# Performance work log

Measured on AMD Instinct MI355X. Metric: run time of the kernel, lower is better.

Reference implementation:

```python
import jax, jax.numpy as jnp
import numpy as np

NEG_BIG = -9.0e15  # matches torch's -9000000000000000.0 mask fill
ALPHA = 0.2        # leakyrelu negative slope


def setup_inputs() -> dict:
    key = jax.random.key(0)
    k1, k2, k3, k4, k5 = jax.random.split(key, 5)
    N, F_in, F_out = 4096, 512, 64
    stdv = 1.0 / np.sqrt(F_out)
    x = jax.random.normal(k1, (N, F_in), dtype=jnp.float32)
    adj = jax.random.randint(k2, (N, N), 0, 2, dtype=jnp.int32)
    W = jax.random.uniform(k3, (F_in, F_out), dtype=jnp.float32, minval=-stdv, maxval=stdv)
    a = jax.random.normal(k4, (2 * F_out, 1), dtype=jnp.float32) * 0.1
    bias = jax.random.uniform(k5, (F_out,), dtype=jnp.float32, minval=-stdv, maxval=stdv)
    return {"x": x, "adj": adj, "W": W, "a": a, "bias": bias}


def _gat_forward(x, adj, W, a, bias):
    N = x.shape[0]
    F_out = W.shape[1]
    h = x @ W  # (N, F)
    a1 = a[:F_out, 0]   # weights hitting the first concat half
    a2 = a[F_out:, 0]   # weights hitting the second concat half
    # First half: row k=i*N+j of the concat holds h_j  ->  e1[j] = h_j . a1
    e1 = h @ a1  # (N,)
    # Second half of this repo's concat is NOT h_i; exact index algebra:
    # second[k=i*N+j, r] = h[(r*N+i)//F, (((r*N+i)%F)*N + j) % F]
    # Since it depends on j only via j % F, build table T[i, t] (t = j % F).
    r = jnp.arange(F_out)[:, None]          # (F, 1)
    i = jnp.arange(N)[None, :]              # (1, N)
    m = r * N + i                           # (F, N)
    p = m // F_out                          # row index into h
    s0 = m % F_out
    t = jnp.arange(F_out)                   # (F,)
    col = (s0[..., None] * N + t) % F_out   # (F, N, F) column index into h
    vals = h[p[..., None], col]             # (F, N, F)
    T = jnp.einsum('r,rit->it', a2, vals)   # (N, F)
    j = jnp.arange(N)
    e2 = T[:, j % F_out]                    # (N, N) second-half contribution
    e = e1[None, :] + e2                    # (N, N) pre-activation scores
    e = jnp.where(e > 0, e, ALPHA * e)      # LeakyReLU(0.2)
    e = jnp.where(adj > 0, e, NEG_BIG)      # mask non-edges
    att = jax.nn.softmax(e, axis=1)         # row-wise softmax (dropout = eval identity)
    out = jax.nn.relu(att @ h) + bias       # relu BEFORE bias add, as in source
    return out


def reference(x, adj, W, a, bias):
    return _gat_forward(x, adj, W, a, bias)
```

## Files before the change

kernel.cpp:

```cpp
#include <hip/hip_runtime.h>
#include <math.h>

#define N_NODES 4096
#define F_IN    512
#define F_OUT   64
#define ALPHA   0.2f
#define NPART   8

typedef _Float16 half8 __attribute__((ext_vector_type(8)));
typedef _Float16 half4 __attribute__((ext_vector_type(4)));
typedef float    floatx4 __attribute__((ext_vector_type(4)));

union H8U4 { half8 h; uint32_t u[4]; };

__device__ __forceinline__ void async_copy16(void* lds, const void* g) {
    __builtin_amdgcn_global_load_lds(
        (const __attribute__((address_space(1))) unsigned int*)g,
        (__attribute__((address_space(3))) unsigned int*)lds, 16, 0, 0);
}

__global__ __launch_bounds__(256) void k_prep(const float* __restrict__ W,
                                              _Float16* __restrict__ WT) {
    int idx = blockIdx.x * 256 + threadIdx.x;
    int t = idx >> 9;
    int k = idx & 511;
    WT[idx] = (_Float16)W[k * F_OUT + t];
}

__global__ __launch_bounds__(512) void k_hW(const float* __restrict__ x,
                                            const _Float16* __restrict__ WT,
                                            const float* __restrict__ a,
                                            float* __restrict__ h,
                                            _Float16* __restrict__ hT,
                                            float* __restrict__ e1) {
    __shared__ float red[8][16][64];
    int tid  = threadIdx.x;
    int lane = tid & 63;
    int w    = tid >> 6;
    int i0   = blockIdx.x * 16;
    int n    = lane & 15;
    int quad = lane >> 4;

    floatx4 acc[4] = {{0,0,0,0},{0,0,0,0},{0,0,0,0},{0,0,0,0}};

    const float* xr = x + (size_t)(i0 + n) * F_IN + w * 64 + quad * 8;
    const _Float16* wb = WT + w * 64 + quad * 8;
#pragma unroll
    for (int kk = 0; kk < 64; kk += 32) {
        float4 x0 = *(const float4*)(xr + kk);
        float4 x1 = *(const float4*)(xr + kk + 4);
        half8 af = {(_Float16)x0.x, (_Float16)x0.y, (_Float16)x0.z, (_Float16)x0.w,
                    (_Float16)x1.x, (_Float16)x1.y, (_Float16)x1.z, (_Float16)x1.w};
#pragma unroll
        for (int g = 0; g < 4; ++g) {
            half8 bf = *(const half8*)(wb + (size_t)(g * 16 + n) * F_IN + kk);
            acc[g] = __builtin_amdgcn_mfma_f32_16x16x32_f16(af, bf, acc[g], 0, 0, 0);
        }
    }
#pragma unroll
    for (int g = 0; g < 4; ++g)
#pragma unroll
        for (int r = 0; r < 4; ++r)
            red[w][g * 4 + r][lane] = acc[g][r];
    __syncthreads();
    if (w != 0) return;
#pragma unroll
    for (int g = 0; g < 4; ++g)
#pragma unroll
        for (int r = 0; r < 4; ++r) {
            float v = 0.f;
#pragma unroll
            for (int ww = 0; ww < 8; ++ww)
                v += red[ww][g * 4 + r][lane];
            acc[g][r] = v;
        }
#pragma unroll
    for (int g = 0; g < 4; ++g) {
        half4 hv;
#pragma unroll
        for (int r = 0; r < 4; ++r) {
            h[(size_t)(i0 + quad * 4 + r) * F_OUT + g * 16 + n] = acc[g][r];
            hv[r] = (_Float16)acc[g][r];
        }
        *(half4*)(hT + (size_t)(g * 16 + n) * N_NODES + i0 + quad * 4) = hv;
    }
    float a1v[4];
#pragma unroll
    for (int g = 0; g < 4; ++g) a1v[g] = a[g * 16 + n];
#pragma unroll
    for (int r = 0; r < 4; ++r) {
        float v = acc[0][r] * a1v[0] + acc[1][r] * a1v[1] + acc[2][r] * a1v[2] + acc[3][r] * a1v[3];
        v += __shfl_xor(v, 1, 64);
        v += __shfl_xor(v, 2, 64);
        v += __shfl_xor(v, 4, 64);
        v += __shfl_xor(v, 8, 64);
        if (n == 0) e1[i0 + quad * 4 + r] = v;
    }
}

__global__ __launch_bounds__(256, 3) void k_main(const int* __restrict__ adj,
                                                 const float* __restrict__ h,
                                                 const float* __restrict__ e1,
                                                 const float* __restrict__ a,
                                                 const _Float16* __restrict__ hT,
                                                 float* __restrict__ out_part,
                                                 float* __restrict__ den_part) {
    __shared__ int      lds_adj[4][8][256];
    __shared__ _Float16 lds_B[16][512];
    __shared__ _Float16 lds_P[512];
    __shared__ float    lds_part[4][64];
    __shared__ float    TqS[64];

    int tid  = threadIdx.x;
    int lane = tid & 63;
    int w    = tid >> 6;
    int b    = blockIdx.x;
    int rb   = b >> 3;
    int s    = b & 7;
    int i0   = rb * 64 + w * 16;
    int n    = lane & 15;
    int quad = lane >> 4;

    {
        int t  = tid & 63;
        int rp = tid >> 6;
        const float* a2 = a + F_OUT;
        float ssum = 0.f;
#pragma unroll
        for (int rr = 0; rr < 16; ++rr) {
            int r = rp * 16 + rr;
            ssum += a2[r] * h[(size_t)r * 4096 + rb * 64 + t];
        }
        lds_part[rp][t] = ssum;
    }
    __syncthreads();
    if (tid < 64)
        TqS[tid] = lds_part[0][tid] + lds_part[1][tid] + lds_part[2][tid] + lds_part[3][tid];
    __syncthreads();
    {
        int j = s * 512 + tid * 2;
        float2 ev = *(const float2*)(e1 + j);
        float e0 = ev.x + TqS[(tid * 2) & 63];
        float e1v = ev.y + TqS[(tid * 2 + 1) & 63];
        e0  = e0  > 0.f ? e0  : ALPHA * e0;
        e1v = e1v > 0.f ? e1v : ALPHA * e1v;
        lds_P[tid * 2]     = (_Float16)__expf(e0);
        lds_P[tid * 2 + 1] = (_Float16)__expf(e1v);
    }

    floatx4 acc[4] = {{0,0,0,0},{0,0,0,0},{0,0,0,0},{0,0,0,0}};
    floatx4 accd = {0, 0, 0, 0};
    _Float16 one_h = (n == 0) ? (_Float16)1.0f : (_Float16)0.0f;
    half8 ones_f = {one_h, one_h, one_h, one_h, one_h, one_h, one_h, one_h};

    for (int it = 0; it < 4; ++it) {
        int jb = s * 512 + it * 128;
        const int* adj_base = adj + (size_t)(i0 + n) * N_NODES + jb + quad * 8;
#pragma unroll
        for (int c = 0; c < 4; ++c) {
            async_copy16(&lds_adj[w][c * 2 + 0][0], adj_base + c * 32);
            async_copy16(&lds_adj[w][c * 2 + 1][0], adj_base + c * 32 + 4);
        }
        const _Float16* hT_base = hT + (size_t)(w * 16 + n) * N_NODES + jb + quad * 8;
#pragma unroll
        for (int c = 0; c < 4; ++c)
            async_copy16(&lds_B[w * 4 + c][0], hT_base + c * 32);
        __syncthreads();

#pragma unroll
        for (int c = 0; c < 4; ++c) {
            int4 ga = *(const int4*)&lds_adj[w][c * 2 + 0][lane * 4];
            int4 gb = *(const int4*)&lds_adj[w][c * 2 + 1][lane * 4];
            H8U4 pv, af;
            pv.h = *(const half8*)&lds_P[it * 128 + c * 32 + quad * 8];
            af.u[0] = pv.u[0] & ((ga.x > 0 ? 0x0000FFFFu : 0u) | (ga.y > 0 ? 0xFFFF0000u : 0u));
            af.u[1] = pv.u[1] & ((ga.z > 0 ? 0x0000FFFFu : 0u) | (ga.w > 0 ? 0xFFFF0000u : 0u));
            af.u[2] = pv.u[2] & ((gb.x > 0 ? 0x0000FFFFu : 0u) | (gb.y > 0 ? 0xFFFF0000u : 0u));
            af.u[3] = pv.u[3] & ((gb.z > 0 ? 0x0000FFFFu : 0u) | (gb.w > 0 ? 0xFFFF0000u : 0u));
#pragma unroll
            for (int g4 = 0; g4 < 4; ++g4) {
                half8 bf = *(const half8*)&lds_B[g4 * 4 + c][lane * 8];
                acc[g4] = __builtin_amdgcn_mfma_f32_16x16x32_f16(af.h, bf, acc[g4], 0, 0, 0);
            }
            accd = __builtin_amdgcn_mfma_f32_16x16x32_f16(af.h, ones_f, accd, 0, 0, 0);
        }
        __syncthreads();
    }

    float* op = out_part + ((size_t)s * N_NODES + i0) * F_OUT;
#pragma unroll
    for (int g4 = 0; g4 < 4; ++g4)
#pragma unroll
        for (int r = 0; r < 4; ++r)
            op[(quad * 4 + r) * F_OUT + g4 * 16 + n] = acc[g4][r];
    if (n == 0) {
#pragma unroll
        for (int r = 0; r < 4; ++r)
            den_part[s * N_NODES + i0 + quad * 4 + r] = accd[r];
    }
}

__global__ __launch_bounds__(128) void k_out(const float* __restrict__ out_part,
                                             const float* __restrict__ den_part,
                                             const float* __restrict__ bias,
                                             float* __restrict__ out) {
    int idx4 = blockIdx.x * 128 + threadIdx.x;
    int base = idx4 * 4;
    int i = base >> 6;
    int t = base & 63;
    float4 sacc = {0.f, 0.f, 0.f, 0.f};
    float dacc = 0.f;
#pragma unroll
    for (int p = 0; p < NPART; ++p) {
        float4 v = ((const float4*)(out_part + (size_t)p * N_NODES * F_OUT))[idx4];
        sacc.x += v.x; sacc.y += v.y; sacc.z += v.z; sacc.w += v.w;
        dacc += den_part[p * N_NODES + i];
    }
    float4 bv = *(const float4*)(bias + t);
    float4 o;
    o.x = fmaxf(sacc.x / dacc, 0.f) + bv.x;
    o.y = fmaxf(sacc.y / dacc, 0.f) + bv.y;
    o.z = fmaxf(sacc.z / dacc, 0.f) + bv.z;
    o.w = fmaxf(sacc.w / dacc, 0.f) + bv.w;
    ((float4*)out)[idx4] = o;
}

extern "C" void kernel_launch(void* const* d_in, const int* in_sizes, int n_in,
                              void* d_out, int out_size, void* d_ws, size_t ws_size,
                              hipStream_t stream) {
    const float* x    = (const float*)d_in[0];
    const int*   adj  = (const int*)d_in[1];
    const float* W    = (const float*)d_in[2];
    const float* a    = (const float*)d_in[3];
    const float* bias = (const float*)d_in[4];
    float* out = (float*)d_out;

    char* ws = (char*)d_ws;
    float*    h        = (float*)ws;
    _Float16* hT       = (_Float16*)(ws + 1024 * 1024);
    float*    e1       = (float*)(ws + 1536 * 1024);
    _Float16* WT       = (_Float16*)(ws + 1552 * 1024);
    float*    out_part = (float*)(ws + 2128 * 1024);
    float*    den_part = (float*)(ws + (2128 + 8192) * 1024);

    k_prep<<<128, 256, 0, stream>>>(W, WT);
    k_hW  <<<256, 512, 0, stream>>>(x, WT, a, h, hT, e1);
    k_main<<<512, 256, 0, stream>>>(adj, h, e1, a, hT, out_part, den_part);
    k_out <<<512, 128, 0, stream>>>(out_part, den_part, bias, out);
}
```

Measured before the change: 120.5 us.

## Double-buffer adj and hT LDS tiles with async prefetch in main loop

Replaces the single-buffered 128-column loop with an 8-step loop over 64-column tiles. Each step issues the next tile's global-to-LDS async loads into the other buffer before computing on the current one, using explicit vmcnt waits and raw barriers. The first tile's load is issued before the attention-score prologue so it overlaps that setup. The goal is to hide global load latency behind MFMA work, at the cost of more barriers and hand-counted waitcnt values that must match the number of outstanding loads.

After: 121.7 us. No clear change (+1.0%).

```diff
diff --git a/kernel.cpp b/kernel.cpp
--- a/kernel.cpp
+++ b/kernel.cpp
@@ -105,8 +105,8 @@
                                                  const _Float16* __restrict__ hT,
                                                  float* __restrict__ out_part,
                                                  float* __restrict__ den_part) {
-    __shared__ int      lds_adj[4][8][256];
-    __shared__ _Float16 lds_B[16][512];
+    __shared__ int      lds_adj[2][4][4][256];
+    __shared__ _Float16 lds_B[2][8][512];
     __shared__ _Float16 lds_P[512];
     __shared__ float    lds_part[4][64];
     __shared__ float    TqS[64];
@@ -120,6 +120,21 @@
     int i0   = rb * 64 + w * 16;
     int n    = lane & 15;
     int quad = lane >> 4;
+
+#define STAGE(t) do {                                                              \
+        const int bf_ = (t) & 1;                                                   \
+        const int jb_ = s * 512 + (t) * 64;                                        \
+        const int* ab_ = adj + (size_t)(i0 + n) * N_NODES + jb_ + quad * 8;        \
+        async_copy16(&lds_adj[bf_][w][0][0], ab_);                                 \
+        async_copy16(&lds_adj[bf_][w][1][0], ab_ + 4);                             \
+        async_copy16(&lds_adj[bf_][w][2][0], ab_ + 32);                            \
+        async_copy16(&lds_adj[bf_][w][3][0], ab_ + 36);                            \
+        const _Float16* hb_ = hT + (size_t)(w * 16 + n) * N_NODES + jb_ + quad * 8;\
+        async_copy16(&lds_B[bf_][w * 2 + 0][0], hb_);                              \
+        async_copy16(&lds_B[bf_][w * 2 + 1][0], hb_ + 32);                         \
+    } while (0)
+
+    STAGE(0);
 
     {
         int t  = tid & 63;
@@ -153,39 +168,39 @@
     _Float16 one_h = (n == 0) ? (_Float16)1.0f : (_Float16)0.0f;
     half8 ones_f = {one_h, one_h, one_h, one_h, one_h, one_h, one_h, one_h};
 
-    for (int it = 0; it < 4; ++it) {
-        int jb = s * 512 + it * 128;
-        const int* adj_base = adj + (size_t)(i0 + n) * N_NODES + jb + quad * 8;
-#pragma unroll
-        for (int c = 0; c < 4; ++c) {
-            async_copy16(&lds_adj[w][c * 2 + 0][0], adj_base + c * 32);
-            async_copy16(&lds_adj[w][c * 2 + 1][0], adj_base + c * 32 + 4);
-        }
-        const _Float16* hT_base = hT + (size_t)(w * 16 + n) * N_NODES + jb + quad * 8;
-#pragma unroll
-        for (int c = 0; c < 4; ++c)
-            async_copy16(&lds_B[w * 4 + c][0], hT_base + c * 32);
-        __syncthreads();
-
-#pragma unroll
-        for (int c = 0; c < 4; ++c) {
-            int4 ga = *(const int4*)&lds_adj[w][c * 2 + 0][lane * 4];
-            int4 gb = *(const int4*)&lds_adj[w][c * 2 + 1][lane * 4];
+#pragma unroll
+    for (int it = 0; it < 8; ++it) {
+        if (it < 7) {
+            STAGE(it + 1);
+            asm volatile("s_waitcnt vmcnt(6) lgkmcnt(0)" ::: "memory");
+        } else {
+            asm volatile("s_waitcnt vmcnt(0) lgkmcnt(0)" ::: "memory");
+        }
+        __builtin_amdgcn_s_barrier();
+        __builtin_amdgcn_sched_barrier(0);
+
+        const int buf = it & 1;
+#pragma unroll
+        for (int c = 0; c < 2; ++c) {
+            int4 ga = *(const int4*)&lds_adj[buf][w][c * 2 + 0][lane * 4];
+            int4 gb = *(const int4*)&lds_adj[buf][w][c * 2 + 1][lane * 4];
             H8U4 pv, af;
-            pv.h = *(const half8*)&lds_P[it * 128 + c * 32 + quad * 8];
+            pv.h = *(const half8*)&lds_P[it * 64 + c * 32 + quad * 8];
             af.u[0] = pv.u[0] & ((ga.x > 0 ? 0x0000FFFFu : 0u) | (ga.y > 0 ? 0xFFFF0000u : 0u));
             af.u[1] = pv.u[1] & ((ga.z > 0 ? 0x0000FFFFu : 0u) | (ga.w > 0 ? 0xFFFF0000u : 0u));
             af.u[2] = pv.u[2] & ((gb.x > 0 ? 0x0000FFFFu : 0u) | (gb.y > 0 ? 0xFFFF0000u : 0u));
             af.u[3] = pv.u[3] & ((gb.z > 0 ? 0x0000FFFFu : 0u) | (gb.w > 0 ? 0xFFFF0000u : 0u));
 #pragma unroll
             for (int g4 = 0; g4 < 4; ++g4) {
-                half8 bf = *(const half8*)&lds_B[g4 * 4 + c][lane * 8];
+                half8 bf = *(const half8*)&lds_B[buf][g4 * 2 + c][lane * 8];
                 acc[g4] = __builtin_amdgcn_mfma_f32_16x16x32_f16(af.h, bf, acc[g4], 0, 0, 0);
             }
             accd = __builtin_amdgcn_mfma_f32_16x16x32_f16(af.h, ones_f, accd, 0, 0, 0);
         }
-        __syncthreads();
-    }
+        __builtin_amdgcn_sched_barrier(0);
+        __builtin_amdgcn_s_barrier();
+    }
+#undef STAGE
 
     float* op = out_part + ((size_t)s * N_NODES + i0) * F_OUT;
 #pragma unroll
```

## Fuse partial reduction into main GAT kernel with double-buffered async staging

Applied to the files above, without the earlier changes.

Drops the W-transpose prep kernel so k_hW reads and converts W directly. It also replaces the 8-way column-split main kernel plus separate reduction kernel with one 512-thread block per 16 rows. Each of the 8 waves covers a 512-column slice and streams adj and hT through double-buffered async LDS copies with explicit vmcnt waits. Partial sums are reduced in shared memory and normalized in place, which removes two launches and the out_part round trip through global memory. The cost is fewer blocks (256), higher LDS use per block, and strided uncoalesced W loads in k_hW.

New measurement: 130.3 us. 8.2% more time.

```diff
diff --git a/kernel.cpp b/kernel.cpp
--- a/kernel.cpp
+++ b/kernel.cpp
@@ -5,7 +5,6 @@
 #define F_IN    512
 #define F_OUT   64
 #define ALPHA   0.2f
-#define NPART   8
 
 typedef _Float16 half8 __attribute__((ext_vector_type(8)));
 typedef _Float16 half4 __attribute__((ext_vector_type(4)));
@@ -19,16 +18,8 @@
         (__attribute__((address_space(3))) unsigned int*)lds, 16, 0, 0);
 }
 
-__global__ __launch_bounds__(256) void k_prep(const float* __restrict__ W,
-                                              _Float16* __restrict__ WT) {
-    int idx = blockIdx.x * 256 + threadIdx.x;
-    int t = idx >> 9;
-    int k = idx & 511;
-    WT[idx] = (_Float16)W[k * F_OUT + t];
-}
-
 __global__ __launch_bounds__(512) void k_hW(const float* __restrict__ x,
-                                            const _Float16* __restrict__ WT,
+                                            const float* __restrict__ W,
                                             const float* __restrict__ a,
                                             float* __restrict__ h,
                                             _Float16* __restrict__ hT,
@@ -44,16 +35,18 @@
     floatx4 acc[4] = {{0,0,0,0},{0,0,0,0},{0,0,0,0},{0,0,0,0}};
 
     const float* xr = x + (size_t)(i0 + n) * F_IN + w * 64 + quad * 8;
-    const _Float16* wb = WT + w * 64 + quad * 8;
 #pragma unroll
     for (int kk = 0; kk < 64; kk += 32) {
         float4 x0 = *(const float4*)(xr + kk);
         float4 x1 = *(const float4*)(xr + kk + 4);
         half8 af = {(_Float16)x0.x, (_Float16)x0.y, (_Float16)x0.z, (_Float16)x0.w,
                     (_Float16)x1.x, (_Float16)x1.y, (_Float16)x1.z, (_Float16)x1.w};
+        int k0 = w * 64 + kk + quad * 8;
 #pragma unroll
         for (int g = 0; g < 4; ++g) {
-            half8 bf = *(const half8*)(wb + (size_t)(g * 16 + n) * F_IN + kk);
+            const float* wc = W + (size_t)k0 * F_OUT + g * 16 + n;
+            half8 bf = {(_Float16)wc[0 * 64], (_Float16)wc[1 * 64], (_Float16)wc[2 * 64], (_Float16)wc[3 * 64],
+                        (_Float16)wc[4 * 64], (_Float16)wc[5 * 64], (_Float16)wc[6 * 64], (_Float16)wc[7 * 64]};
             acc[g] = __builtin_amdgcn_mfma_f32_16x16x32_f16(af, bf, acc[g], 0, 0, 0);
         }
     }
@@ -98,131 +91,147 @@
     }
 }
 
-__global__ __launch_bounds__(256, 3) void k_main(const int* __restrict__ adj,
-                                                 const float* __restrict__ h,
-                                                 const float* __restrict__ e1,
-                                                 const float* __restrict__ a,
-                                                 const _Float16* __restrict__ hT,
-                                                 float* __restrict__ out_part,
-                                                 float* __restrict__ den_part) {
-    __shared__ int      lds_adj[4][8][256];
-    __shared__ _Float16 lds_B[16][512];
-    __shared__ _Float16 lds_P[512];
-    __shared__ float    lds_part[4][64];
-    __shared__ float    TqS[64];
+union ShM {
+    struct {
+        int      adjS[8][2][2][256];
+        _Float16 BS[8][2][4][512];
+    } st;
+    struct {
+        float red[8][16][64];
+    } rd;
+};
+
+__global__ __launch_bounds__(512, 2) void k_main2(const int* __restrict__ adj,
+                                                  const float* __restrict__ h,
+                                                  const float* __restrict__ e1,
+                                                  const float* __restrict__ a,
+                                                  const _Float16* __restrict__ hT,
+                                                  const float* __restrict__ bias,
+                                                  float* __restrict__ out) {
+    __shared__ ShM shm;
+    __shared__ _Float16 P[4096];
+    __shared__ float part[8][64];
+    __shared__ float Tq[64];
 
     int tid  = threadIdx.x;
     int lane = tid & 63;
     int w    = tid >> 6;
     int b    = blockIdx.x;
-    int rb   = b >> 3;
-    int s    = b & 7;
-    int i0   = rb * 64 + w * 16;
+    int i0   = b * 16;
+    int rbq  = b >> 2;
     int n    = lane & 15;
     int quad = lane >> 4;
+
+#define STG(t_) do {                                                                \
+        const int bf_ = (t_) & 1;                                                   \
+        const int j0_ = w * 512 + (t_) * 32;                                        \
+        const int* ab_ = adj + (size_t)(i0 + n) * N_NODES + j0_ + quad * 4;         \
+        async_copy16(&shm.st.adjS[w][bf_][0][0], ab_);                              \
+        async_copy16(&shm.st.adjS[w][bf_][1][0], ab_ + 16);                         \
+        const _Float16* hb_ = hT + (size_t)n * N_NODES + j0_ + quad * 8;            \
+        async_copy16(&shm.st.BS[w][bf_][0][0], hb_);                                \
+        async_copy16(&shm.st.BS[w][bf_][1][0], hb_ + 16 * N_NODES);                 \
+        async_copy16(&shm.st.BS[w][bf_][2][0], hb_ + 32 * N_NODES);                 \
+        async_copy16(&shm.st.BS[w][bf_][3][0], hb_ + 48 * N_NODES);                 \
+    } while (0)
+
+    STG(0);
 
     {
         int t  = tid & 63;
         int rp = tid >> 6;
         const float* a2 = a + F_OUT;
-        float ssum = 0.f;
-#pragma unroll
-        for (int rr = 0; rr < 16; ++rr) {
-            int r = rp * 16 + rr;
-            ssum += a2[r] * h[(size_t)r * 4096 + rb * 64 + t];
-        }
-        lds_part[rp][t] = ssum;
+        float ss = 0.f;
+#pragma unroll
+        for (int rr = 0; rr < 8; ++rr) {
+            int r = rp * 8 + rr;
+            ss += a2[r] * h[(size_t)r * 4096 + rbq * 64 + t];
+        }
+        part[rp][t] = ss;
     }
     __syncthreads();
     if (tid < 64)
-        TqS[tid] = lds_part[0][tid] + lds_part[1][tid] + lds_part[2][tid] + lds_part[3][tid];
+        Tq[tid] = part[0][tid] + part[1][tid] + part[2][tid] + part[3][tid]
+                + part[4][tid] + part[5][tid] + part[6][tid] + part[7][tid];
     __syncthreads();
     {
-        int j = s * 512 + tid * 2;
-        float2 ev = *(const float2*)(e1 + j);
-        float e0 = ev.x + TqS[(tid * 2) & 63];
-        float e1v = ev.y + TqS[(tid * 2 + 1) & 63];
-        e0  = e0  > 0.f ? e0  : ALPHA * e0;
-        e1v = e1v > 0.f ? e1v : ALPHA * e1v;
-        lds_P[tid * 2]     = (_Float16)__expf(e0);
-        lds_P[tid * 2 + 1] = (_Float16)__expf(e1v);
-    }
+        int j8 = tid * 8;
+        float4 ev0 = *(const float4*)(e1 + j8);
+        float4 ev1 = *(const float4*)(e1 + j8 + 4);
+        float ev[8] = {ev0.x, ev0.y, ev0.z, ev0.w, ev1.x, ev1.y, ev1.z, ev1.w};
+        half8 ph;
+#pragma unroll
+        for (int u = 0; u < 8; ++u) {
+            float val = ev[u] + Tq[(j8 + u) & 63];
+            val = val > 0.f ? val : ALPHA * val;
+            ph[u] = (_Float16)__expf(val);
+        }
+        *(half8*)&P[j8] = ph;
+    }
+    __syncthreads();
 
     floatx4 acc[4] = {{0,0,0,0},{0,0,0,0},{0,0,0,0},{0,0,0,0}};
     floatx4 accd = {0, 0, 0, 0};
     _Float16 one_h = (n == 0) ? (_Float16)1.0f : (_Float16)0.0f;
     half8 ones_f = {one_h, one_h, one_h, one_h, one_h, one_h, one_h, one_h};
 
-    for (int it = 0; it < 4; ++it) {
-        int jb = s * 512 + it * 128;
-        const int* adj_base = adj + (size_t)(i0 + n) * N_NODES + jb + quad * 8;
-#pragma unroll
-        for (int c = 0; c < 4; ++c) {
-            async_copy16(&lds_adj[w][c * 2 + 0][0], adj_base + c * 32);
-            async_copy16(&lds_adj[w][c * 2 + 1][0], adj_base + c * 32 + 4);
-        }
-        const _Float16* hT_base = hT + (size_t)(w * 16 + n) * N_NODES + jb + quad * 8;
-#pragma unroll
-        for (int c = 0; c < 4; ++c)
-            async_copy16(&lds_B[w * 4 + c][0], hT_base + c * 32);
-        __syncthreads();
-
-#pragma unroll
-        for (int c = 0; c < 4; ++c) {
-            int4 ga = *(const int4*)&lds_adj[w][c * 2 + 0][lane * 4];
-            int4 gb = *(const int4*)&lds_adj[w][c * 2 + 1][lane * 4];
-            H8U4 pv, af;
-            pv.h = *(const half8*)&lds_P[it * 128 + c * 32 + quad * 8];
-            af.u[0] = pv.u[0] & ((ga.x > 0 ? 0x0000FFFFu : 0u) | (ga.y > 0 ? 0xFFFF0000u : 0u));
-            af.u[1] = pv.u[1] & ((ga.z > 0 ? 0x0000FFFFu : 0u) | (ga.w > 0 ? 0xFFFF0000u : 0u));
-            af.u[2] = pv.u[2] & ((gb.x > 0 ? 0x0000FFFFu : 0u) | (gb.y > 0 ? 0xFFFF0000u : 0u));
-            af.u[3] = pv.u[3] & ((gb.z > 0 ? 0x0000FFFFu : 0u) | (gb.w > 0 ? 0xFFFF0000u : 0u));
-#pragma unroll
-            for (int g4 = 0; g4 < 4; ++g4) {
-                half8 bf = *(const half8*)&lds_B[g4 * 4 + c][lane * 8];
-                acc[g4] = __builtin_amdgcn_mfma_f32_16x16x32_f16(af.h, bf, acc[g4], 0, 0, 0);
-            }
-            accd = __builtin_amdgcn_mfma_f32_16x16x32_f16(af.h, ones_f, accd, 0, 0, 0);
-        }
-        __syncthreads();
-    }
-
-    float* op = out_part + ((size_t)s * N_NODES + i0) * F_OUT;
+    const int ia = (((2 * quad) & 3) * 16 + n) * 4;
+    const int ib = (((2 * quad + 1) & 3) * 16 + n) * 4;
+    const int cq = quad >> 1;
+
+#pragma unroll 2
+    for (int st = 0; st < 16; ++st) {
+        if (st < 15) {
+            STG(st + 1);
+            asm volatile("s_waitcnt vmcnt(6)" ::: "memory");
+        } else {
+            asm volatile("s_waitcnt vmcnt(0)" ::: "memory");
+        }
+        __builtin_amdgcn_sched_barrier(0);
+
+        const int buf = st & 1;
+        const int j0  = w * 512 + st * 32;
+        int4 ga = *(const int4*)&shm.st.adjS[w][buf][cq][ia];
+        int4 gb = *(const int4*)&shm.st.adjS[w][buf][cq][ib];
+        H8U4 pv, af;
+        pv.h = *(const half8*)&P[j0 + quad * 8];
+        af.u[0] = pv.u[0] & ((ga.x > 0 ? 0x0000FFFFu : 0u) | (ga.y > 0 ? 0xFFFF0000u : 0u));
+        af.u[1] = pv.u[1] & ((ga.z > 0 ? 0x0000FFFFu : 0u) | (ga.w > 0 ? 0xFFFF0000u : 0u));
+        af.u[2] = pv.u[2] & ((gb.x > 0 ? 0x0000FFFFu : 0u) | (gb.y > 0 ? 0xFFFF0000u : 0u));
+        af.u[3] = pv.u[3] & ((gb.z > 0 ? 0x0000FFFFu : 0u) | (gb.w > 0 ? 0xFFFF0000u : 0u));
+#pragma unroll
+        for (int g4 = 0; g4 < 4; ++g4) {
+            half8 bf = *(const half8*)&shm.st.BS[w][buf][g4][lane * 8];
+            acc[g4] = __builtin_amdgcn_mfma_f32_16x16x32_f16(af.h, bf, acc[g4], 0, 0, 0);
+        }
+        accd = __builtin_amdgcn_mfma_f32_16x16x32_f16(af.h, ones_f, accd, 0, 0, 0);
+    }
+#undef STG
+
 #pragma unroll
     for (int g4 = 0; g4 < 4; ++g4)
 #pragma unroll
         for (int r = 0; r < 4; ++r)
-            op[(quad * 4 + r) * F_OUT + g4 * 16 + n] = acc[g4][r];
+            shm.rd.red[w][quad * 4 + r][g4 * 16 + n] = acc[g4][r];
     if (n == 0) {
 #pragma unroll
         for (int r = 0; r < 4; ++r)
-            den_part[s * N_NODES + i0 + quad * 4 + r] = accd[r];
-    }
-}
-
-__global__ __launch_bounds__(128) void k_out(const float* __restrict__ out_part,
-                                             const float* __restrict__ den_part,
-                                             const float* __restrict__ bias,
-                                             float* __restrict__ out) {
-    int idx4 = blockIdx.x * 128 + threadIdx.x;
-    int base = idx4 * 4;
-    int i = base >> 6;
-    int t = base & 63;
-    float4 sacc = {0.f, 0.f, 0.f, 0.f};
-    float dacc = 0.f;
-#pragma unroll
-    for (int p = 0; p < NPART; ++p) {
-        float4 v = ((const float4*)(out_part + (size_t)p * N_NODES * F_OUT))[idx4];
-        sacc.x += v.x; sacc.y += v.y; sacc.z += v.z; sacc.w += v.w;
-        dacc += den_part[p * N_NODES + i];
-    }
-    float4 bv = *(const float4*)(bias + t);
-    float4 o;
-    o.x = fmaxf(sacc.x / dacc, 0.f) + bv.x;
-    o.y = fmaxf(sacc.y / dacc, 0.f) + bv.y;
-    o.z = fmaxf(sacc.z / dacc, 0.f) + bv.z;
-    o.w = fmaxf(sacc.w / dacc, 0.f) + bv.w;
-    ((float4*)out)[idx4] = o;
+            part[w][quad * 4 + r] = accd[r];
+    }
+    __syncthreads();
+
+#pragma unroll
+    for (int e = tid; e < 1024; e += 512) {
+        int row = e >> 6;
+        int t   = e & 63;
+        float num = 0.f, den = 0.f;
+#pragma unroll
+        for (int ww = 0; ww < 8; ++ww) {
+            num += shm.rd.red[ww][row][t];
+            den += part[ww][row];
+        }
+        out[(size_t)(i0 + row) * F_OUT + t] = fmaxf(num / den, 0.f) + bias[t];
+    }
 }
 
 extern "C" void kernel_launch(void* const* d_in, const int* in_sizes, int n_in,
@@ -236,15 +245,10 @@
     float* out = (float*)d_out;
 
     char* ws = (char*)d_ws;
-    float*    h        = (float*)ws;
-    _Float16* hT       = (_Float16*)(ws + 1024 * 1024);
-    float*    e1       = (float*)(ws + 1536 * 1024);
-    _Float16* WT       = (_Float16*)(ws + 1552 * 1024);
-    float*    out_part = (float*)(ws + 2128 * 1024);
-    float*    den_part = (float*)(ws + (2128 + 8192) * 1024);
-
-    k_prep<<<128, 256, 0, stream>>>(W, WT);
-    k_hW  <<<256, 512, 0, stream>>>(x, WT, a, h, hT, e1);
-    k_main<<<512, 256, 0, stream>>>(adj, h, e1, a, hT, out_part, den_part);
-    k_out <<<512, 128, 0, stream>>>(out_part, den_part, bias, out);
-}
+    float*    h  = (float*)ws;
+    _Float16* hT = (_Float16*)(ws + 1024 * 1024);
+    float*    e1 = (float*)(ws + 1536 * 1024);
+
+    k_hW   <<<256, 512, 0, stream>>>(x, W, a, h, hT, e1);
+    k_main2<<<256, 512, 0, stream>>>(adj, h, e1, a, hT, bias, out);
+}
```

## Double-buffer adj/hT LDS staging and split columns into 16 partitions

Applied to the files above, without the earlier changes.

The main kernel now splits the column range into 16 partitions instead of 8, launching twice as many blocks with a smaller LDS footprint and requesting 4 waves per SIMD. The adjacency and hT tiles are streamed in 32-column stages through a two-slot LDS buffer, prefetching the next stage with async copies while the current stage runs MFMA. Explicit vmcnt waits and barriers replace the old load-all-then-sync loop. This aims to hide global load latency and raise occupancy, at the cost of doubling the partial output buffers that the final reduction kernel must read and sum.

Result: slower. 123.5 us (+2.5%).

```diff
diff --git a/kernel.cpp b/kernel.cpp
--- a/kernel.cpp
+++ b/kernel.cpp
@@ -5,7 +5,7 @@
 #define F_IN    512
 #define F_OUT   64
 #define ALPHA   0.2f
-#define NPART   8
+#define NPART   16
 
 typedef _Float16 half8 __attribute__((ext_vector_type(8)));
 typedef _Float16 half4 __attribute__((ext_vector_type(4)));
@@ -98,16 +98,16 @@
     }
 }
 
-__global__ __launch_bounds__(256, 3) void k_main(const int* __restrict__ adj,
+__global__ __launch_bounds__(256, 4) void k_main(const int* __restrict__ adj,
                                                  const float* __restrict__ h,
                                                  const float* __restrict__ e1,
                                                  const float* __restrict__ a,
                                                  const _Float16* __restrict__ hT,
                                                  float* __restrict__ out_part,
                                                  float* __restrict__ den_part) {
-    __shared__ int      lds_adj[4][8][256];
-    __shared__ _Float16 lds_B[16][512];
-    __shared__ _Float16 lds_P[512];
+    __shared__ int      lds_adj[4][2][2][256];
+    __shared__ _Float16 lds_B[4][2][16][32];
+    __shared__ _Float16 lds_P[256];
     __shared__ float    lds_part[4][64];
     __shared__ float    TqS[64];
 
@@ -115,11 +115,24 @@
     int lane = tid & 63;
     int w    = tid >> 6;
     int b    = blockIdx.x;
-    int rb   = b >> 3;
-    int s    = b & 7;
+    int rb   = b >> 4;
+    int s    = b & 15;
     int i0   = rb * 64 + w * 16;
     int n    = lane & 15;
     int quad = lane >> 4;
+
+#define STG(t_) do {                                                                    \
+        const int bf_ = (t_) & 1;                                                       \
+        const int jb_ = s * 256 + (t_) * 32;                                            \
+        const int* ab_ = adj + (size_t)(i0 + n) * N_NODES + jb_ + quad * 8;             \
+        async_copy16(&lds_adj[w][bf_][0][0], ab_);                                      \
+        async_copy16(&lds_adj[w][bf_][1][0], ab_ + 4);                                  \
+        const _Float16* hb_ = hT + (size_t)(w * 16 + (lane >> 2)) * N_NODES             \
+                                 + jb_ + (lane & 3) * 8;                                \
+        async_copy16(&lds_B[w][bf_][0][0], hb_);                                        \
+    } while (0)
+
+    STG(0);
 
     {
         int t  = tid & 63;
@@ -138,54 +151,49 @@
         TqS[tid] = lds_part[0][tid] + lds_part[1][tid] + lds_part[2][tid] + lds_part[3][tid];
     __syncthreads();
     {
-        int j = s * 512 + tid * 2;
-        float2 ev = *(const float2*)(e1 + j);
-        float e0 = ev.x + TqS[(tid * 2) & 63];
-        float e1v = ev.y + TqS[(tid * 2 + 1) & 63];
-        e0  = e0  > 0.f ? e0  : ALPHA * e0;
-        e1v = e1v > 0.f ? e1v : ALPHA * e1v;
-        lds_P[tid * 2]     = (_Float16)__expf(e0);
-        lds_P[tid * 2 + 1] = (_Float16)__expf(e1v);
-    }
+        int j = s * 256 + tid;
+        float e0 = e1[j] + TqS[tid & 63];
+        e0 = e0 > 0.f ? e0 : ALPHA * e0;
+        lds_P[tid] = (_Float16)__expf(e0);
+    }
+    __syncthreads();
 
     floatx4 acc[4] = {{0,0,0,0},{0,0,0,0},{0,0,0,0},{0,0,0,0}};
     floatx4 accd = {0, 0, 0, 0};
     _Float16 one_h = (n == 0) ? (_Float16)1.0f : (_Float16)0.0f;
     half8 ones_f = {one_h, one_h, one_h, one_h, one_h, one_h, one_h, one_h};
 
-    for (int it = 0; it < 4; ++it) {
-        int jb = s * 512 + it * 128;
-        const int* adj_base = adj + (size_t)(i0 + n) * N_NODES + jb + quad * 8;
-#pragma unroll
-        for (int c = 0; c < 4; ++c) {
-            async_copy16(&lds_adj[w][c * 2 + 0][0], adj_base + c * 32);
-            async_copy16(&lds_adj[w][c * 2 + 1][0], adj_base + c * 32 + 4);
-        }
-        const _Float16* hT_base = hT + (size_t)(w * 16 + n) * N_NODES + jb + quad * 8;
-#pragma unroll
-        for (int c = 0; c < 4; ++c)
-            async_copy16(&lds_B[w * 4 + c][0], hT_base + c * 32);
-        __syncthreads();
-
-#pragma unroll
-        for (int c = 0; c < 4; ++c) {
-            int4 ga = *(const int4*)&lds_adj[w][c * 2 + 0][lane * 4];
-            int4 gb = *(const int4*)&lds_adj[w][c * 2 + 1][lane * 4];
-            H8U4 pv, af;
-            pv.h = *(const half8*)&lds_P[it * 128 + c * 32 + quad * 8];
-            af.u[0] = pv.u[0] & ((ga.x > 0 ? 0x0000FFFFu : 0u) | (ga.y > 0 ? 0xFFFF0000u : 0u));
-            af.u[1] = pv.u[1] & ((ga.z > 0 ? 0x0000FFFFu : 0u) | (ga.w > 0 ? 0xFFFF0000u : 0u));
-            af.u[2] = pv.u[2] & ((gb.x > 0 ? 0x0000FFFFu : 0u) | (gb.y > 0 ? 0xFFFF0000u : 0u));
-            af.u[3] = pv.u[3] & ((gb.z > 0 ? 0x0000FFFFu : 0u) | (gb.w > 0 ? 0xFFFF0000u : 0u));
-#pragma unroll
-            for (int g4 = 0; g4 < 4; ++g4) {
-                half8 bf = *(const half8*)&lds_B[g4 * 4 + c][lane * 8];
-                acc[g4] = __builtin_amdgcn_mfma_f32_16x16x32_f16(af.h, bf, acc[g4], 0, 0, 0);
-            }
-            accd = __builtin_amdgcn_mfma_f32_16x16x32_f16(af.h, ones_f, accd, 0, 0, 0);
-        }
-        __syncthreads();
-    }
+#pragma unroll
+    for (int st = 0; st < 8; ++st) {
+        if (st < 7) {
+            STG(st + 1);
+            asm volatile("s_waitcnt vmcnt(3)" ::: "memory");
+        } else {
+            asm volatile("s_waitcnt vmcnt(0)" ::: "memory");
+        }
+        __builtin_amdgcn_s_barrier();
+        __builtin_amdgcn_sched_barrier(0);
+
+        const int buf = st & 1;
+        int4 ga = *(const int4*)&lds_adj[w][buf][0][(quad * 16 + n) * 4];
+        int4 gb = *(const int4*)&lds_adj[w][buf][1][(quad * 16 + n) * 4];
+        H8U4 pv, af;
+        pv.h = *(const half8*)&lds_P[st * 32 + quad * 8];
+        af.u[0] = pv.u[0] & ((ga.x > 0 ? 0x0000FFFFu : 0u) | (ga.y > 0 ? 0xFFFF0000u : 0u));
+        af.u[1] = pv.u[1] & ((ga.z > 0 ? 0x0000FFFFu : 0u) | (ga.w > 0 ? 0xFFFF0000u : 0u));
+        af.u[2] = pv.u[2] & ((gb.x > 0 ? 0x0000FFFFu : 0u) | (gb.y > 0 ? 0xFFFF0000u : 0u));
+        af.u[3] = pv.u[3] & ((gb.z > 0 ? 0x0000FFFFu : 0u) | (gb.w > 0 ? 0xFFFF0000u : 0u));
+#pragma unroll
+        for (int g4 = 0; g4 < 4; ++g4) {
+            half8 bf = *(const half8*)&lds_B[g4][buf][n][quad * 8];
+            acc[g4] = __builtin_amdgcn_mfma_f32_16x16x32_f16(af.h, bf, acc[g4], 0, 0, 0);
+        }
+        accd = __builtin_amdgcn_mfma_f32_16x16x32_f16(af.h, ones_f, accd, 0, 0, 0);
+
+        __builtin_amdgcn_sched_barrier(0);
+        __builtin_amdgcn_s_barrier();
+    }
+#undef STG
 
     float* op = out_part + ((size_t)s * N_NODES + i0) * F_OUT;
 #pragma unroll
@@ -241,10 +249,10 @@
     float*    e1       = (float*)(ws + 1536 * 1024);
     _Float16* WT       = (_Float16*)(ws + 1552 * 1024);
     float*    out_part = (float*)(ws + 2128 * 1024);
-    float*    den_part = (float*)(ws + (2128 + 8192) * 1024);
+    float*    den_part = (float*)(ws + (2128 + 16384) * 1024);
 
     k_prep<<<128, 256, 0, stream>>>(W, WT);
     k_hW  <<<256, 512, 0, stream>>>(x, WT, a, h, hT, e1);
-    k_main<<<512, 256, 0, stream>>>(adj, h, e1, a, hT, out_part, den_part);
+    k_main<<<1024, 256, 0, stream>>>(adj, h, e1, a, hT, out_part, den_part);
     k_out <<<512, 128, 0, stream>>>(out_part, den_part, bias, out);
 }
```
